# Kernel tuning notes

Hardware: AMD Instinct MI355X
Metric: run time of the kernel (lower is better)

## Reference

```python
import jax, jax.numpy as jnp
import numpy as np

D = 4544
H = 71
DKV = 64  # D // H
NKV = 1   # multi-query: one shared KV head
ROPE_BASE = 10000.0


def setup_inputs() -> dict:
    key = jax.random.key(0)
    k1, k2, k3 = jax.random.split(key, 3)
    N, L = 2, 1024
    hidden_states = jax.random.normal(k1, (N, L, D), dtype=jnp.float32)
    W_qkv = jax.random.normal(k2, (D + 2 * NKV * DKV, D), dtype=jnp.float32) * (D ** -0.5)
    W_dense = jax.random.normal(k3, (D, D), dtype=jnp.float32) * (D ** -0.5)
    return {"hidden_states": hidden_states, "W_qkv": W_qkv, "W_dense": W_dense}


def _rope_cos_sin(L, dtype):
    inv_freq = 1.0 / (ROPE_BASE ** (jnp.arange(0, DKV, 2, dtype=jnp.float32) / DKV))  # [Dkv/2]
    t = jnp.arange(L, dtype=jnp.float32)
    freqs = jnp.outer(t, inv_freq)                 # [L, Dkv/2]
    emb = jnp.concatenate((freqs, freqs), axis=1)  # [L, Dkv]
    cos = jnp.cos(emb)[None, None, :, :].astype(dtype)  # [1,1,L,Dkv]
    sin = jnp.sin(emb)[None, None, :, :].astype(dtype)
    return cos, sin


def _rotate_half(x):
    half = x.shape[-1] // 2
    return jnp.concatenate((-x[..., half:], x[..., :half]), axis=-1)


def reference(hidden_states, W_qkv, W_dense):
    N, L, _ = hidden_states.shape
    # Fused QKV projection (no bias): [N, L, D + 2*Dkv]
    fused = jnp.einsum('nld,ed->nle', hidden_states, W_qkv)
    fused = fused.reshape(N, L, H + 2 * NKV, DKV)
    query = jnp.transpose(fused[:, :, : H, :], (0, 2, 1, 3))            # [N, H, L, Dkv]
    key_h = jnp.transpose(fused[:, :, H : H + NKV, :], (0, 2, 1, 3))    # [N, 1, L, Dkv]
    value = jnp.transpose(fused[:, :, H + NKV :, :], (0, 2, 1, 3))      # [N, 1, L, Dkv]

    # RoPE (prefill path: positions 0..L-1)
    cos, sin = _rope_cos_sin(L, query.dtype)
    query = query * cos + _rotate_half(query) * sin
    key_h = key_h * cos + _rotate_half(key_h) * sin

    # Causal SDPA with multi-query KV broadcast (scale = 1/sqrt(Dkv))
    k = key_h[:, 0]    # [N, L, Dkv]
    v = value[:, 0]    # [N, L, Dkv]
    scale = 1.0 / jnp.sqrt(jnp.asarray(DKV, dtype=query.dtype))
    scores = jnp.einsum('nhqd,nkd->nhqk', query, k) * scale  # [N, H, L, L]
    causal = jnp.tril(jnp.ones((L, L), dtype=bool))
    scores = jnp.where(causal[None, None], scores, jnp.finfo(scores.dtype).min)
    weights = jax.nn.softmax(scores, axis=-1)
    attn = jnp.einsum('nhqk,nkd->nhqd', weights, v)           # [N, H, L, Dkv]

    attn = jnp.transpose(attn, (0, 2, 1, 3)).reshape(N, L, H * DKV)  # [N, L, D]
    out = jnp.einsum('nld,ed->nle', attn, W_dense)
    return out
```

## Files before the change

kernel.cpp:

```cpp
#include <hip/hip_runtime.h>

#define D_MODEL 4544
#define E_QKV   4672
#define E_STR   4736
#define E_PAD2  4864
#define D_PAD   4608
#define NH      71
#define SEQ     1024
#define NB      2
#define M_ROWS  2048

typedef __bf16 bf16_t;
typedef bf16_t bf16x8 __attribute__((ext_vector_type(8)));
typedef float f32x4 __attribute__((ext_vector_type(4)));
typedef float f32x16 __attribute__((ext_vector_type(16)));
typedef unsigned u32x4 __attribute__((ext_vector_type(4)));

typedef __attribute__((address_space(1))) const void* gas_ptr;
typedef __attribute__((address_space(3))) void* las_ptr;

static __device__ __forceinline__ unsigned short f2bf(float f) {
  union { float f; unsigned u; } v; v.f = f;
  unsigned r = (v.u + 0x7fffu + ((v.u >> 16) & 1u)) >> 16;
  return (unsigned short)r;
}

static __device__ __forceinline__ unsigned cvtpk_bf16(float lo, float hi) {
  unsigned r;
  asm("v_cvt_pk_bf16_f32 %0, %1, %2" : "=v"(r) : "v"(lo), "v"(hi));
  return r;
}

static __device__ __forceinline__ float fast_exp2(float x) {
  float r;
  asm("v_exp_f32 %0, %1" : "=v"(r) : "v"(x));
  return r;
}

__global__ void convert_pad(const float* __restrict__ src, unsigned short* __restrict__ dst,
                            int rows_src, int rows_pad, int cols) {
  int idx = blockIdx.x * 256 + threadIdx.x;
  int cols4 = cols >> 2;
  int total = rows_pad * cols4;
  if (idx >= total) return;
  int row = idx / cols4;
  int c4 = (idx - row * cols4) << 2;
  ushort4 o;
  if (row < rows_src) {
    const float4 v = *(const float4*)(src + (size_t)row * cols + c4);
    o.x = f2bf(v.x); o.y = f2bf(v.y); o.z = f2bf(v.z); o.w = f2bf(v.w);
  } else {
    o.x = 0; o.y = 0; o.z = 0; o.w = 0;
  }
  *(ushort4*)(dst + (size_t)row * cols + c4) = o;
}

#define REGION(b_, op_, kh_) (((((b_)*2+(op_))*2)+(kh_)) << 13)

#define STAGE(b_, op_, kh_, kt_) do {                                          \
  const unsigned short* _p0 = (op_) ? pB0 : pA0;                               \
  const unsigned short* _p1 = (op_) ? pB1 : pA1;                               \
  const int _koff = ((kt_) << 6) + ((kh_) << 5);                               \
  __builtin_amdgcn_global_load_lds((gas_ptr)(_p0 + _koff),                     \
      (las_ptr)(lds + REGION(b_, op_, kh_) + (wave << 9)), 16, 0, 0);          \
  __builtin_amdgcn_global_load_lds((gas_ptr)(_p1 + _koff),                     \
      (las_ptr)(lds + REGION(b_, op_, kh_) + ((8 + wave) << 9)), 16, 0, 0);    \
} while (0)

#define LDA4(b_, kh_, mh_) do {                                                \
  const unsigned short* _ab = lds + REGION(b_, 0, kh_);                        \
  _Pragma("unroll")                                                            \
  for (int _mm = 0; _mm < 4; ++_mm)                                            \
    a[_mm] = *(const bf16x8*)&_ab[((wm * 8 + (mh_) * 4 + _mm) << 9) + lane * 8]; \
} while (0)

#define LDB4(b_, kh_) do {                                                     \
  const unsigned short* _bp = lds + REGION(b_, 1, kh_);                        \
  _Pragma("unroll")                                                            \
  for (int _n = 0; _n < 4; ++_n)                                               \
    bv[_n] = *(const bf16x8*)&_bp[((wn * 4 + _n) << 9) + lane * 8];            \
} while (0)

#define MFMA16(mh_) do {                                                       \
  _Pragma("unroll")                                                            \
  for (int _mm = 0; _mm < 4; ++_mm)                                            \
    _Pragma("unroll")                                                          \
    for (int _n = 0; _n < 4; ++_n)                                             \
      acc[(mh_) * 4 + _mm][_n] = __builtin_amdgcn_mfma_f32_16x16x32_bf16(      \
          a[_mm], bv[_n], acc[(mh_) * 4 + _mm][_n], 0, 0, 0);                  \
} while (0)

__global__ __launch_bounds__(512, 2) void gemm256(
    const unsigned short* __restrict__ A,
    const unsigned short* __restrict__ B,
    float* __restrict__ C0, float* __restrict__ C1, float* __restrict__ C2,
    int K, int Ntiles, int ldc, int Nact, int chunk) {
  __shared__ __align__(16) unsigned short lds[65536];
  const int tid = threadIdx.x;
  const int wave = tid >> 6, lane = tid & 63;
  const int g = lane >> 4, c = lane & 15;
  const int wm = wave >> 2, wn = wave & 3;
  const int nwg = gridDim.x;
  const int swz = (blockIdx.x & 7) * (nwg >> 3) + (blockIdx.x >> 3);
  const int tilesTot = 8 * Ntiles;
  const int kc = swz / tilesTot;
  const int tile = swz - kc * tilesTot;
  const int bm = tile / Ntiles, bn = tile - bm * Ntiles;
  const size_t bRow = (size_t)bm * 256, bCol = (size_t)bn * 256;
  const int NTtot = K >> 6;
  const int kb = kc * chunk;
  const int nt = (NTtot - kb < chunk) ? (NTtot - kb) : chunk;
  float* __restrict__ C = (kc == 0) ? C0 : ((kc == 1) ? C1 : C2);

  const unsigned short* pA0 = A + (bRow + (size_t)(wave * 16 + c)) * K + g * 8;
  const unsigned short* pA1 = A + (bRow + (size_t)((8 + wave) * 16 + c)) * K + g * 8;
  const unsigned short* pB0 = B + (bCol + (size_t)(wave * 16 + c)) * K + g * 8;
  const unsigned short* pB1 = B + (bCol + (size_t)((8 + wave) * 16 + c)) * K + g * 8;

  f32x4 acc[8][4] = {};

  STAGE(0, 0, 0, kb); STAGE(0, 1, 0, kb); STAGE(0, 0, 1, kb); STAGE(0, 1, 1, kb);
  STAGE(1, 1, 0, kb + 1); STAGE(1, 0, 0, kb + 1); STAGE(1, 1, 1, kb + 1);
  asm volatile("s_waitcnt vmcnt(6)" ::: "memory");
  __builtin_amdgcn_s_barrier();

  for (int t = 0; t < nt; ++t) {
    const int b = t & 1;
    const int tn1 = kb + ((t + 1 < nt) ? t + 1 : 0);
    const int tn2 = kb + ((t + 2 < nt) ? t + 2 : 0);
    bf16x8 a[4], bv[4];
    LDA4(b, 0, 0); LDB4(b, 0);
    STAGE(b ^ 1, 0, 1, tn1);
    __builtin_amdgcn_s_barrier();
    asm volatile("s_waitcnt lgkmcnt(0)" ::: "memory");
    __builtin_amdgcn_s_setprio(1);
    MFMA16(0);
    __builtin_amdgcn_s_setprio(0);
    __builtin_amdgcn_s_barrier();
    LDA4(b, 0, 1);
    STAGE(b, 1, 0, tn2);
    __builtin_amdgcn_s_barrier();
    asm volatile("s_waitcnt lgkmcnt(0)" ::: "memory");
    __builtin_amdgcn_s_setprio(1);
    MFMA16(1);
    __builtin_amdgcn_s_setprio(0);
    __builtin_amdgcn_s_barrier();
    LDA4(b, 1, 0); LDB4(b, 1);
    STAGE(b, 0, 0, tn2);
    __builtin_amdgcn_s_barrier();
    asm volatile("s_waitcnt lgkmcnt(0)" ::: "memory");
    __builtin_amdgcn_s_setprio(1);
    MFMA16(0);
    __builtin_amdgcn_s_setprio(0);
    __builtin_amdgcn_s_barrier();
    LDA4(b, 1, 1);
    STAGE(b, 1, 1, tn2);
    __builtin_amdgcn_s_barrier();
    asm volatile("s_waitcnt lgkmcnt(0)" ::: "memory");
    __builtin_amdgcn_s_setprio(1);
    MFMA16(1);
    __builtin_amdgcn_s_setprio(0);
    asm volatile("s_waitcnt vmcnt(6)" ::: "memory");
    __builtin_amdgcn_s_barrier();
  }
  asm volatile("s_waitcnt vmcnt(0)" ::: "memory");

#pragma unroll
  for (int mm = 0; mm < 8; ++mm) {
#pragma unroll
    for (int n = 0; n < 4; ++n) {
      int col = (int)bCol + wn * 64 + n * 16 + c;
      if (col < Nact) {
#pragma unroll
        for (int r = 0; r < 4; ++r) {
          size_t row = bRow + wm * 128 + mm * 16 + g * 4 + r;
          C[row * ldc + col] = acc[mm][n][r];
        }
      }
    }
  }
}

__global__ void reduce3(const float* __restrict__ p0, const float* __restrict__ p1,
                        const float* __restrict__ p2, float* __restrict__ out, int total4) {
  int idx = blockIdx.x * 256 + threadIdx.x;
  if (idx >= total4) return;
  float4 a = *(const float4*)(p0 + (size_t)idx * 4);
  float4 b = *(const float4*)(p1 + (size_t)idx * 4);
  float4 cc = *(const float4*)(p2 + (size_t)idx * 4);
  float4 o;
  o.x = a.x + b.x + cc.x; o.y = a.y + b.y + cc.y;
  o.z = a.z + b.z + cc.z; o.w = a.w + b.w + cc.w;
  *(float4*)(out + (size_t)idx * 4) = o;
}

__global__ void rope_extract(const float* __restrict__ p0, const float* __restrict__ p1,
                             const float* __restrict__ p2, int np,
                             unsigned short* __restrict__ Qb,
                             unsigned short* __restrict__ Kb,
                             unsigned short* __restrict__ VTb) {
  int idx = blockIdx.x * 256 + threadIdx.x;
  const int total = NB * SEQ * 73 * 64;
  if (idx >= total) return;
  int d = idx & 63;
  int t = idx >> 6;
  int h = t % 73;  t /= 73;
  int l = t & (SEQ - 1);
  int n = t >> 10;
  const size_t base = ((size_t)(n * SEQ + l)) * E_STR + h * 64;
  float x = p0[base + d];
  if (np == 3) x += p1[base + d] + p2[base + d];
  if (h == 72) {
    VTb[((size_t)(n * 64 + d)) * SEQ + l] = f2bf(x);
    return;
  }
  int dh = d & 31;
  float inv = __expf(-(float)dh * (9.210340371976184f / 32.0f));
  float ang = (float)l * inv;
  float sn, cs;
  __sincosf(ang, &sn, &cs);
  int dx = (d < 32) ? d + 32 : d - 32;
  float xr = p0[base + dx];
  if (np == 3) xr += p1[base + dx] + p2[base + dx];
  float rh = (d < 32) ? -xr : xr;
  float out = x * cs + rh * sn;
  if (h == 71) {
    Kb[((size_t)(n * SEQ + l)) * 64 + d] = f2bf(out);
  } else {
    Qb[(((size_t)(n * NH + h)) * SEQ + l) * 64 + d] = f2bf(out * 0.1803368801111204f);
  }
}

#define LOADK(dst_, ktv_) do {                                                 \
  _Pragma("unroll")                                                            \
  for (int _cc = 0; _cc < 4; ++_cc) {                                          \
    dst_[_cc]     = *(const bf16x8*)&kbase[(size_t)((ktv_) + c) * 64 + _cc * 16 + hi * 8];      \
    dst_[4 + _cc] = *(const bf16x8*)&kbase[(size_t)((ktv_) + 32 + c) * 64 + _cc * 16 + hi * 8]; \
  }                                                                            \
} while (0)

__global__ __launch_bounds__(128) void attn_kernel(
    const unsigned short* __restrict__ Qb,
    const unsigned short* __restrict__ Kb,
    const unsigned short* __restrict__ VTb,
    unsigned short* __restrict__ attnb) {
  const int h = blockIdx.y, n = blockIdx.z;
  const int wave = threadIdx.x >> 6, lane = threadIdx.x & 63;
  const int c = lane & 31, hi = lane >> 5;
  const int gw = blockIdx.x * 2 + wave;

  const unsigned short* kbase = Kb + (size_t)n * SEQ * 64;
  const unsigned short* vtbase = VTb + (size_t)n * 64 * SEQ;

  for (int pass = 0; pass < 2; ++pass) {
    const int tile = pass ? gw : (31 - gw);
    const int qrow0 = tile * 32;
    const int q = qrow0 + c;
    const int nk = qrow0 + 32;
    const unsigned short* qbase = Qb + (((size_t)(n * NH + h)) * SEQ + qrow0) * 64;

    bf16x8 qf[4];
#pragma unroll
    for (int cc = 0; cc < 4; ++cc)
      qf[cc] = *(const bf16x8*)&qbase[c * 64 + cc * 16 + hi * 8];

    f32x16 o0 = {}, o1 = {};
    float m_run = -1e30f, l_run = 0.f;

    bf16x8 kc[8], kn[8];
    LOADK(kc, 0);

    for (int kt = 0; kt < nk; kt += 64) {
      const bool more = (kt + 64) < nk;
      f32x16 s0 = {}, s1 = {};
#pragma unroll
      for (int cc = 0; cc < 4; ++cc) {
        s0 = __builtin_amdgcn_mfma_f32_32x32x16_bf16(kc[cc], qf[cc], s0, 0, 0, 0);
        s1 = __builtin_amdgcn_mfma_f32_32x32x16_bf16(kc[4 + cc], qf[cc], s1, 0, 0, 0);
      }
      if (more) LOADK(kn, kt + 64);
      bf16x8 vv0[4], vv1[4];
#pragma unroll
      for (int cg = 0; cg < 4; ++cg) {
        vv0[cg] = *(const bf16x8*)&vtbase[(size_t)c * SEQ + kt + cg * 16 + hi * 8];
        vv1[cg] = *(const bf16x8*)&vtbase[(size_t)(32 + c) * SEQ + kt + cg * 16 + hi * 8];
      }
      __builtin_amdgcn_sched_barrier(0);
      if (kt + 63 > qrow0) {
#pragma unroll
        for (int r = 0; r < 16; ++r) {
          const int key0 = kt + (r & 3) + 8 * (r >> 2) + 4 * hi;
          s0[r] = (key0 > q) ? -1e30f : s0[r];
          s1[r] = (key0 + 32 > q) ? -1e30f : s1[r];
        }
      }
      float tt[16];
#pragma unroll
      for (int r = 0; r < 16; ++r) tt[r] = fmaxf(s0[r], s1[r]);
#pragma unroll
      for (int st = 8; st > 0; st >>= 1)
#pragma unroll
        for (int r = 0; r < 8; ++r) if (r < st) tt[r] = fmaxf(tt[r], tt[r + st]);
      float mx = fmaxf(tt[0], __shfl_xor(tt[0], 32));
      const float mnew = fmaxf(m_run, mx);
      const float aa = fast_exp2(m_run - mnew);
#pragma unroll
      for (int r = 0; r < 16; ++r) {
        s0[r] = fast_exp2(s0[r] - mnew);
        s1[r] = fast_exp2(s1[r] - mnew);
      }
      float ps = 0.f;
#pragma unroll
      for (int r = 0; r < 16; ++r) ps += s0[r] + s1[r];
      ps += __shfl_xor(ps, 32);
      l_run = l_run * aa + ps;
      m_run = mnew;
#pragma unroll
      for (int r = 0; r < 16; ++r) { o0[r] *= aa; o1[r] *= aa; }

#pragma unroll
      for (int half = 0; half < 2; ++half) {
#pragma unroll
        for (int ccl = 0; ccl < 2; ++ccl) {
          const int cg = half * 2 + ccl;
          unsigned a0, a1, b0, b1;
          if (half == 0) {
            a0 = cvtpk_bf16(s0[8 * ccl + 0], s0[8 * ccl + 1]);
            a1 = cvtpk_bf16(s0[8 * ccl + 2], s0[8 * ccl + 3]);
            b0 = cvtpk_bf16(s0[8 * ccl + 4], s0[8 * ccl + 5]);
            b1 = cvtpk_bf16(s0[8 * ccl + 6], s0[8 * ccl + 7]);
          } else {
            a0 = cvtpk_bf16(s1[8 * ccl + 0], s1[8 * ccl + 1]);
            a1 = cvtpk_bf16(s1[8 * ccl + 2], s1[8 * ccl + 3]);
            b0 = cvtpk_bf16(s1[8 * ccl + 4], s1[8 * ccl + 5]);
            b1 = cvtpk_bf16(s1[8 * ccl + 6], s1[8 * ccl + 7]);
          }
          unsigned xa0 = __shfl_xor(a0, 32), xa1 = __shfl_xor(a1, 32);
          unsigned xb0 = __shfl_xor(b0, 32), xb1 = __shfl_xor(b1, 32);
          u32x4 fw;
          fw[0] = hi ? xb0 : a0;
          fw[1] = hi ? xb1 : a1;
          fw[2] = hi ? b0 : xa0;
          fw[3] = hi ? b1 : xa1;
          union { u32x4 u; bf16x8 b; } pf; pf.u = fw;
          o0 = __builtin_amdgcn_mfma_f32_32x32x16_bf16(vv0[cg], pf.b, o0, 0, 0, 0);
          o1 = __builtin_amdgcn_mfma_f32_32x32x16_bf16(vv1[cg], pf.b, o1, 0, 0, 0);
        }
      }
      if (more) {
#pragma unroll
        for (int cc = 0; cc < 8; ++cc) kc[cc] = kn[cc];
      }
    }

    const float inv = 1.0f / l_run;
    const size_t rowoff = (size_t)(n * SEQ + q) * D_MODEL + h * 64;
#pragma unroll
    for (int rr = 0; rr < 4; ++rr) {
      ushort4 w0, w1;
      w0.x = f2bf(o0[4 * rr + 0] * inv); w0.y = f2bf(o0[4 * rr + 1] * inv);
      w0.z = f2bf(o0[4 * rr + 2] * inv); w0.w = f2bf(o0[4 * rr + 3] * inv);
      w1.x = f2bf(o1[4 * rr + 0] * inv); w1.y = f2bf(o1[4 * rr + 1] * inv);
      w1.z = f2bf(o1[4 * rr + 2] * inv); w1.w = f2bf(o1[4 * rr + 3] * inv);
      *(ushort4*)&attnb[rowoff + 8 * rr + 4 * hi] = w0;
      *(ushort4*)&attnb[rowoff + 32 + 8 * rr + 4 * hi] = w1;
    }
  }
}

extern "C" void kernel_launch(void* const* d_in, const int* in_sizes, int n_in,
                              void* d_out, int out_size, void* d_ws, size_t ws_size,
                              hipStream_t stream) {
  const float* hs = (const float*)d_in[0];
  const float* wqkv = (const float*)d_in[1];
  const float* wdense = (const float*)d_in[2];
  float* out = (float*)d_out;
  char* ws = (char*)d_ws;

  unsigned short* hsb   = (unsigned short*)(ws + 0);
  unsigned short* wqkvb = (unsigned short*)(ws + 18612224);
  unsigned short* wdb   = (unsigned short*)(ws + 62820352);
  float*          fused = (float*)(ws + 104701952);
  unsigned short* qb    = (unsigned short*)(ws + 143499264);
  unsigned short* kb    = (unsigned short*)(ws + 162111488);
  unsigned short* vtb   = (unsigned short*)(ws + 162373632);
  unsigned short* attnb = (unsigned short*)(ws + 162635776);
  float* fusedE1 = (float*)(ws + 181248000);
  float* fusedE2 = (float*)(ws + 220045312);
  const int splitOK = (ws_size >= (size_t)258842624) ? 1 : 0;

  {
    int total = M_ROWS * (D_MODEL / 4);
    convert_pad<<<(total + 255) / 256, 256, 0, stream>>>(hs, hsb, M_ROWS, M_ROWS, D_MODEL);
  }
  {
    int total = E_PAD2 * (D_MODEL / 4);
    convert_pad<<<(total + 255) / 256, 256, 0, stream>>>(wqkv, wqkvb, E_QKV, E_PAD2, D_MODEL);
  }
  {
    int total = D_PAD * (D_MODEL / 4);
    convert_pad<<<(total + 255) / 256, 256, 0, stream>>>(wdense, wdb, D_MODEL, D_PAD, D_MODEL);
  }

  if (splitOK) {
    gemm256<<<dim3(8 * 19 * 3), 512, 0, stream>>>(hsb, wqkvb, fused, fusedE1, fusedE2,
                                                  D_MODEL, 19, E_STR, E_STR, 24);
  } else {
    gemm256<<<dim3(8 * 19), 512, 0, stream>>>(hsb, wqkvb, fused, fused, fused,
                                              D_MODEL, 19, E_STR, E_STR, 71);
  }
  {
    int total = NB * SEQ * 73 * 64;
    rope_extract<<<(total + 255) / 256, 256, 0, stream>>>(fused, fusedE1, fusedE2,
                                                          splitOK ? 3 : 1, qb, kb, vtb);
  }
  attn_kernel<<<dim3(8, NH, NB), 128, 0, stream>>>(qb, kb, vtb, attnb);
  if (splitOK) {
    float* p0 = (float*)(ws + 0);
    float* p1 = fused;
    float* p2 = fusedE1;
    gemm256<<<dim3(8 * 18 * 3), 512, 0, stream>>>(attnb, wdb, p0, p1, p2,
                                                  D_MODEL, 18, D_MODEL, D_MODEL, 24);
    int total4 = (M_ROWS * D_MODEL) / 4;
    reduce3<<<(total4 + 255) / 256, 256, 0, stream>>>(p0, p1, p2, out, total4);
  } else {
    gemm256<<<dim3(8 * 18), 512, 0, stream>>>(attnb, wdb, out, out, out,
                                              D_MODEL, 18, D_MODEL, D_MODEL, 71);
  }
}
```

Measured before the change: 433.1 us.

## Switch GEMM to 32x32x16 MFMA tiles and merge three conversion kernels

The GEMM inner loop moves from 16x16x32 bf16 MFMA fragments to 32x32x16 fragments. The LDS staging layout, fragment loads, accumulator shape and output store mapping are rewritten to match. Larger MFMA tiles cut the number of LDS fragment reads per FLOP and the instruction issue overhead. Separately, the three fp32-to-bf16 convert launches are merged into one kernel to save launch overhead. The new output index mapping for 32x32 accumulators must be exactly right or the results will be wrong.

```diff
diff --git a/kernel.cpp b/kernel.cpp
--- a/kernel.cpp
+++ b/kernel.cpp
@@ -37,57 +37,72 @@
   return r;
 }
 
-__global__ void convert_pad(const float* __restrict__ src, unsigned short* __restrict__ dst,
-                            int rows_src, int rows_pad, int cols) {
+__global__ void convert3(const float* __restrict__ hs, const float* __restrict__ wq,
+                         const float* __restrict__ wd,
+                         unsigned short* __restrict__ hsb, unsigned short* __restrict__ wqb,
+                         unsigned short* __restrict__ wdb) {
+  const int C4 = D_MODEL >> 2;
   int idx = blockIdx.x * 256 + threadIdx.x;
-  int cols4 = cols >> 2;
-  int total = rows_pad * cols4;
-  if (idx >= total) return;
-  int row = idx / cols4;
-  int c4 = (idx - row * cols4) << 2;
+  const int n1 = M_ROWS * C4;
+  const int n2 = n1 + E_PAD2 * C4;
+  const int n3 = n2 + D_PAD * C4;
+  if (idx >= n3) return;
+  const float* src; unsigned short* dst; int rows_src; int rel;
+  if (idx < n1)      { src = hs; dst = hsb; rows_src = M_ROWS;  rel = idx; }
+  else if (idx < n2) { src = wq; dst = wqb; rows_src = E_QKV;   rel = idx - n1; }
+  else               { src = wd; dst = wdb; rows_src = D_MODEL; rel = idx - n2; }
+  int row = rel / C4;
+  int c4 = (rel - row * C4) << 2;
   ushort4 o;
   if (row < rows_src) {
-    const float4 v = *(const float4*)(src + (size_t)row * cols + c4);
+    const float4 v = *(const float4*)(src + (size_t)row * D_MODEL + c4);
     o.x = f2bf(v.x); o.y = f2bf(v.y); o.z = f2bf(v.z); o.w = f2bf(v.w);
   } else {
     o.x = 0; o.y = 0; o.z = 0; o.w = 0;
   }
-  *(ushort4*)(dst + (size_t)row * cols + c4) = o;
-}
-
-#define REGION(b_, op_, kh_) (((((b_)*2+(op_))*2)+(kh_)) << 13)
-
-#define STAGE(b_, op_, kh_, kt_) do {                                          \
-  const unsigned short* _p0 = (op_) ? pB0 : pA0;                               \
-  const unsigned short* _p1 = (op_) ? pB1 : pA1;                               \
-  const int _koff = ((kt_) << 6) + ((kh_) << 5);                               \
-  __builtin_amdgcn_global_load_lds((gas_ptr)(_p0 + _koff),                     \
-      (las_ptr)(lds + REGION(b_, op_, kh_) + (wave << 9)), 16, 0, 0);          \
-  __builtin_amdgcn_global_load_lds((gas_ptr)(_p1 + _koff),                     \
-      (las_ptr)(lds + REGION(b_, op_, kh_) + ((8 + wave) << 9)), 16, 0, 0);    \
+  *(ushort4*)(dst + (size_t)row * D_MODEL + c4) = o;
+}
+
+#define REG16(b_, op_) ((((b_) * 2 + (op_)) << 14))
+
+#define STAGE2(b_, op_, ksp_, kt_) do {                                        \
+  const unsigned short* _p = (op_) ? pB : pA;                                  \
+  const int _k0 = ((kt_) << 6) + ((ksp_) << 5);                                \
+  __builtin_amdgcn_global_load_lds((gas_ptr)(_p + _k0),                        \
+      (las_ptr)(lds + REG16(b_, op_) + ((wave * 4 + (ksp_) * 2) << 9)), 16, 0, 0); \
+  __builtin_amdgcn_global_load_lds((gas_ptr)(_p + _k0 + 16),                   \
+      (las_ptr)(lds + REG16(b_, op_) + ((wave * 4 + (ksp_) * 2 + 1) << 9)), 16, 0, 0); \
 } while (0)
 
-#define LDA4(b_, kh_, mh_) do {                                                \
-  const unsigned short* _ab = lds + REGION(b_, 0, kh_);                        \
+#define LDA4(b_, ksp_, mq_) do {                                               \
+  const unsigned short* _ab = lds + REG16(b_, 0);                              \
   _Pragma("unroll")                                                            \
-  for (int _mm = 0; _mm < 4; ++_mm)                                            \
-    a[_mm] = *(const bf16x8*)&_ab[((wm * 8 + (mh_) * 4 + _mm) << 9) + lane * 8]; \
+  for (int _m = 0; _m < 2; ++_m)                                               \
+    _Pragma("unroll")                                                          \
+    for (int _ks = 0; _ks < 2; ++_ks)                                          \
+      a[_m * 2 + _ks] = *(const bf16x8*)&_ab[                                  \
+          (((wm * 4 + (mq_) * 2 + _m) * 4 + (ksp_) * 2 + _ks) << 9) + lane * 8]; \
 } while (0)
 
-#define LDB4(b_, kh_) do {                                                     \
-  const unsigned short* _bp = lds + REGION(b_, 1, kh_);                        \
+#define LDB4(b_, ksp_) do {                                                    \
+  const unsigned short* _bp = lds + REG16(b_, 1);                              \
   _Pragma("unroll")                                                            \
-  for (int _n = 0; _n < 4; ++_n)                                               \
-    bv[_n] = *(const bf16x8*)&_bp[((wn * 4 + _n) << 9) + lane * 8];            \
+  for (int _n = 0; _n < 2; ++_n)                                               \
+    _Pragma("unroll")                                                          \
+    for (int _ks = 0; _ks < 2; ++_ks)                                          \
+      bv[_n * 2 + _ks] = *(const bf16x8*)&_bp[                                 \
+          (((wn * 2 + _n) * 4 + (ksp_) * 2 + _ks) << 9) + lane * 8];           \
 } while (0)
 
-#define MFMA16(mh_) do {                                                       \
+#define MFMA8(mq_) do {                                                        \
   _Pragma("unroll")                                                            \
-  for (int _mm = 0; _mm < 4; ++_mm)                                            \
+  for (int _m = 0; _m < 2; ++_m)                                               \
     _Pragma("unroll")                                                          \
-    for (int _n = 0; _n < 4; ++_n)                                             \
-      acc[(mh_) * 4 + _mm][_n] = __builtin_amdgcn_mfma_f32_16x16x32_bf16(      \
-          a[_mm], bv[_n], acc[(mh_) * 4 + _mm][_n], 0, 0, 0);                  \
+    for (int _n = 0; _n < 2; ++_n)                                             \
+      _Pragma("unroll")                                                        \
+      for (int _ks = 0; _ks < 2; ++_ks)                                        \
+        acc[(mq_) * 2 + _m][_n] = __builtin_amdgcn_mfma_f32_32x32x16_bf16(     \
+            a[_m * 2 + _ks], bv[_n * 2 + _ks], acc[(mq_) * 2 + _m][_n], 0, 0, 0); \
 } while (0)
 
 __global__ __launch_bounds__(512, 2) void gemm256(
@@ -98,7 +113,7 @@
   __shared__ __align__(16) unsigned short lds[65536];
   const int tid = threadIdx.x;
   const int wave = tid >> 6, lane = tid & 63;
-  const int g = lane >> 4, c = lane & 15;
+  const int hi = lane >> 5;
   const int wm = wave >> 2, wn = wave & 3;
   const int nwg = gridDim.x;
   const int swz = (blockIdx.x & 7) * (nwg >> 3) + (blockIdx.x >> 3);
@@ -112,15 +127,13 @@
   const int nt = (NTtot - kb < chunk) ? (NTtot - kb) : chunk;
   float* __restrict__ C = (kc == 0) ? C0 : ((kc == 1) ? C1 : C2);
 
-  const unsigned short* pA0 = A + (bRow + (size_t)(wave * 16 + c)) * K + g * 8;
-  const unsigned short* pA1 = A + (bRow + (size_t)((8 + wave) * 16 + c)) * K + g * 8;
-  const unsigned short* pB0 = B + (bCol + (size_t)(wave * 16 + c)) * K + g * 8;
-  const unsigned short* pB1 = B + (bCol + (size_t)((8 + wave) * 16 + c)) * K + g * 8;
-
-  f32x4 acc[8][4] = {};
-
-  STAGE(0, 0, 0, kb); STAGE(0, 1, 0, kb); STAGE(0, 0, 1, kb); STAGE(0, 1, 1, kb);
-  STAGE(1, 1, 0, kb + 1); STAGE(1, 0, 0, kb + 1); STAGE(1, 1, 1, kb + 1);
+  const unsigned short* pA = A + (bRow + (size_t)(wave * 32 + (lane & 31))) * K + hi * 8;
+  const unsigned short* pB = B + (bCol + (size_t)(wave * 32 + (lane & 31))) * K + hi * 8;
+
+  f32x16 acc[4][2] = {};
+
+  STAGE2(0, 0, 0, kb); STAGE2(0, 1, 0, kb); STAGE2(0, 0, 1, kb); STAGE2(0, 1, 1, kb);
+  STAGE2(1, 1, 0, kb + 1); STAGE2(1, 0, 0, kb + 1); STAGE2(1, 1, 1, kb + 1);
   asm volatile("s_waitcnt vmcnt(6)" ::: "memory");
   __builtin_amdgcn_s_barrier();
 
@@ -130,35 +143,35 @@
     const int tn2 = kb + ((t + 2 < nt) ? t + 2 : 0);
     bf16x8 a[4], bv[4];
     LDA4(b, 0, 0); LDB4(b, 0);
-    STAGE(b ^ 1, 0, 1, tn1);
+    STAGE2(b ^ 1, 0, 1, tn1);
     __builtin_amdgcn_s_barrier();
     asm volatile("s_waitcnt lgkmcnt(0)" ::: "memory");
     __builtin_amdgcn_s_setprio(1);
-    MFMA16(0);
+    MFMA8(0);
     __builtin_amdgcn_s_setprio(0);
     __builtin_amdgcn_s_barrier();
     LDA4(b, 0, 1);
-    STAGE(b, 1, 0, tn2);
+    STAGE2(b, 1, 0, tn2);
     __builtin_amdgcn_s_barrier();
     asm volatile("s_waitcnt lgkmcnt(0)" ::: "memory");
     __builtin_amdgcn_s_setprio(1);
-    MFMA16(1);
+    MFMA8(1);
     __builtin_amdgcn_s_setprio(0);
     __builtin_amdgcn_s_barrier();
     LDA4(b, 1, 0); LDB4(b, 1);
-    STAGE(b, 0, 0, tn2);
+    STAGE2(b, 0, 0, tn2);
     __builtin_amdgcn_s_barrier();
     asm volatile("s_waitcnt lgkmcnt(0)" ::: "memory");
     __builtin_amdgcn_s_setprio(1);
-    MFMA16(0);
+    MFMA8(0);
     __builtin_amdgcn_s_setprio(0);
     __builtin_amdgcn_s_barrier();
     LDA4(b, 1, 1);
-    STAGE(b, 1, 1, tn2);
+    STAGE2(b, 1, 1, tn2);
     __builtin_amdgcn_s_barrier();
     asm volatile("s_waitcnt lgkmcnt(0)" ::: "memory");
     __builtin_amdgcn_s_setprio(1);
-    MFMA16(1);
+    MFMA8(1);
     __builtin_amdgcn_s_setprio(0);
     asm volatile("s_waitcnt vmcnt(6)" ::: "memory");
     __builtin_amdgcn_s_barrier();
@@ -166,15 +179,15 @@
   asm volatile("s_waitcnt vmcnt(0)" ::: "memory");
 
 #pragma unroll
-  for (int mm = 0; mm < 8; ++mm) {
-#pragma unroll
-    for (int n = 0; n < 4; ++n) {
-      int col = (int)bCol + wn * 64 + n * 16 + c;
+  for (int am = 0; am < 4; ++am) {
+#pragma unroll
+    for (int nf = 0; nf < 2; ++nf) {
+      int col = (int)bCol + wn * 64 + nf * 32 + (lane & 31);
       if (col < Nact) {
 #pragma unroll
-        for (int r = 0; r < 4; ++r) {
-          size_t row = bRow + wm * 128 + mm * 16 + g * 4 + r;
-          C[row * ldc + col] = acc[mm][n][r];
+        for (int r = 0; r < 16; ++r) {
+          size_t row = bRow + wm * 128 + am * 32 + (r & 3) + 8 * (r >> 2) + 4 * hi;
+          C[row * ldc + col] = acc[am][nf][r];
         }
       }
     }
@@ -390,16 +403,9 @@
   const int splitOK = (ws_size >= (size_t)258842624) ? 1 : 0;
 
   {
-    int total = M_ROWS * (D_MODEL / 4);
-    convert_pad<<<(total + 255) / 256, 256, 0, stream>>>(hs, hsb, M_ROWS, M_ROWS, D_MODEL);
-  }
-  {
-    int total = E_PAD2 * (D_MODEL / 4);
-    convert_pad<<<(total + 255) / 256, 256, 0, stream>>>(wqkv, wqkvb, E_QKV, E_PAD2, D_MODEL);
-  }
-  {
-    int total = D_PAD * (D_MODEL / 4);
-    convert_pad<<<(total + 255) / 256, 256, 0, stream>>>(wdense, wdb, D_MODEL, D_PAD, D_MODEL);
+    const int C4 = D_MODEL >> 2;
+    int total = (M_ROWS + E_PAD2 + D_PAD) * C4;
+    convert3<<<(total + 255) / 256, 256, 0, stream>>>(hs, wqkv, wdense, hsb, wqkvb, wdb);
   }
 
   if (splitOK) {
```

Result: no change. 441.7 us (+2.0%).
